# Kernel tuning notes

Hardware: AMD Instinct MI355X
Metric: run time of the kernel (lower is better)

The kernel has to match this reference:

```python
import jax, jax.numpy as jnp
import numpy as np

S, M, E = 8192, 4096, 64          # tokens, model_dim, num_experts
CAPACITY_FACTOR = 1.0
MIN_CAPACITY = 8
CAPACITY = max(int(np.ceil(S / E * CAPACITY_FACTOR)), MIN_CAPACITY)  # 128


def setup_inputs() -> dict:
    key = jax.random.key(0)
    k1, k2 = jax.random.split(key)
    x = jax.random.normal(k1, (S, M), dtype=jnp.float32)
    wg = jax.random.normal(k2, (E, M), dtype=jnp.float32) * (1.0 / np.sqrt(M))
    return {"x": x, "wg": wg}


def reference(x, wg):
    # gate projection (Linear, no bias): logits [s, e]
    logits = jnp.einsum('sm,em->se', x, wg)
    gates = jax.nn.softmax(logits, axis=1)                      # [s, e]

    # top-1 expert per token
    indices1_s = jnp.argmax(gates, axis=1)                      # [s]
    mask1 = jax.nn.one_hot(indices1_s, E, dtype=jnp.int32)      # [s, e]
    exp_counts = jnp.sum(mask1, axis=0)                         # [e]

    # load-balancing aux loss
    me = jnp.mean(gates, axis=0)
    ce = jnp.mean(mask1.astype(jnp.float32), axis=0)
    l_aux = jnp.sum(me * ce) * E

    # capacity drop (use_rts=False): keep first CAPACITY tokens per expert.
    # torch: top_idx = topk(mask1, capacity, dim=0)[1]; scatter ones at those rows.
    top_idx = jax.lax.top_k(mask1.T, CAPACITY)[1]               # [e, c] token ids
    keep = jnp.zeros((S, E), dtype=jnp.int32).at[top_idx.T, jnp.arange(E)[None, :]].set(1)
    mask1 = mask1 * keep                                        # [s, e]

    # position of each token inside its expert's buffer
    locations1 = jnp.cumsum(mask1, axis=0) - 1                  # [s, e]
    locations1_s = jnp.sum(locations1 * mask1, axis=1)          # [s]

    mask1_f = mask1.astype(gates.dtype)
    gates_masked = gates * mask1_f                              # [s, e]
    locations1_sc = jax.nn.one_hot(locations1_s, CAPACITY, dtype=jnp.float32)  # [s, c]

    combine_weights = jnp.einsum('se,sc->sec', gates_masked, locations1_sc)    # [s, e, c]
    dispatch_mask = combine_weights.astype(bool)
    return l_aux, combine_weights, dispatch_mask, exp_counts
```

## Files before the change

### kernel.cpp

```cpp
#include <hip/hip_runtime.h>
#include <hip/hip_bf16.h>

#define TS 8192
#define TM 4096
#define TE 64
#define TCAP 128
static const size_t CW = (size_t)TS * TE * TCAP;
static const size_t OUT_ELEMS = 1 + 2 * CW + TE;
static const size_t OUT_BYTES = OUT_ELEMS * sizeof(float);

#define BM 256
#define BK 16
#define SA 260
#define SW 68

__global__ __launch_bounds__(256) void gemm_partial(
    const float* __restrict__ x, const float* __restrict__ wg,
    float* __restrict__ part, int kchunk) {
  __shared__ float As[BK][SA];
  __shared__ float Ws[BK][SW];
  const int tid = threadIdx.x;
  const int t0 = blockIdx.x * BM;
  const int k0 = blockIdx.y * kchunk;
  const int ntile = kchunk / BK;
  const int tg = tid >> 3;
  const int eg = tid & 7;

  float acc[8][8] = {};
  float4 ra[4]; float4 rw;

  auto load_tile = [&](int kt) {
    const int kb = k0 + kt * BK;
#pragma unroll
    for (int i = 0; i < 4; i++) {
      int idx = tid + 256 * i;
      int tok = idx >> 2, c4 = idx & 3;
      ra[i] = *(const float4*)&x[(size_t)(t0 + tok) * TM + kb + 4 * c4];
    }
    int e = tid >> 2, c4 = tid & 3;
    rw = *(const float4*)&wg[(size_t)e * TM + kb + 4 * c4];
  };

  load_tile(0);
  for (int kt = 0; kt < ntile; kt++) {
#pragma unroll
    for (int i = 0; i < 4; i++) {
      int idx = tid + 256 * i;
      int tok = idx >> 2, c4 = idx & 3;
      As[4 * c4 + 0][tok] = ra[i].x; As[4 * c4 + 1][tok] = ra[i].y;
      As[4 * c4 + 2][tok] = ra[i].z; As[4 * c4 + 3][tok] = ra[i].w;
    }
    { int e = tid >> 2, c4 = tid & 3;
      Ws[4 * c4 + 0][e] = rw.x; Ws[4 * c4 + 1][e] = rw.y;
      Ws[4 * c4 + 2][e] = rw.z; Ws[4 * c4 + 3][e] = rw.w; }
    __syncthreads();
    if (kt + 1 < ntile) load_tile(kt + 1);
#pragma unroll
    for (int k = 0; k < BK; k++) {
      float4 a0 = *(const float4*)&As[k][tg * 8];
      float4 a1 = *(const float4*)&As[k][tg * 8 + 4];
      float4 b0 = *(const float4*)&Ws[k][eg * 8];
      float4 b1 = *(const float4*)&Ws[k][eg * 8 + 4];
      float av[8] = {a0.x, a0.y, a0.z, a0.w, a1.x, a1.y, a1.z, a1.w};
      float bv[8] = {b0.x, b0.y, b0.z, b0.w, b1.x, b1.y, b1.z, b1.w};
#pragma unroll
      for (int i = 0; i < 8; i++)
#pragma unroll
        for (int j = 0; j < 8; j++) acc[i][j] += av[i] * bv[j];
    }
    __syncthreads();
  }
  float* dst = part + (size_t)blockIdx.y * TS * TE;
#pragma unroll
  for (int i = 0; i < 8; i++) {
    int tok = t0 + tg * 8 + i;
#pragma unroll
    for (int j = 0; j < 8; j += 4) {
      float4 v = make_float4(acc[i][j], acc[i][j + 1], acc[i][j + 2], acc[i][j + 3]);
      *(float4*)&dst[(size_t)tok * TE + eg * 8 + j] = v;
    }
  }
}

__global__ __launch_bounds__(256) void softmax_top1(
    const float* __restrict__ part, int KS,
    float* __restrict__ gates, float* __restrict__ gate1, int* __restrict__ idx1) {
  const int s = blockIdx.x * 4 + (threadIdx.x >> 6);
  const int lane = threadIdx.x & 63;
  float logit = 0.0f;
  for (int p = 0; p < KS; p++)
    logit += part[((size_t)p * TS + s) * TE + lane];

  float mv = logit; int mi = lane;
#pragma unroll
  for (int off = 32; off; off >>= 1) {
    float ov = __shfl_xor(mv, off);
    int oi = __shfl_xor(mi, off);
    if (ov > mv || (ov == mv && oi < mi)) { mv = ov; mi = oi; }
  }
  float ex = expf(logit - mv);
  float sum = ex;
#pragma unroll
  for (int off = 32; off; off >>= 1) sum += __shfl_xor(sum, off);
  float g = ex / sum;
  gates[(size_t)s * TE + lane] = g;
  if (lane == mi) { gate1[s] = g; idx1[s] = mi; }
}

__global__ __launch_bounds__(256) void me_reduce(const float* __restrict__ gates,
                                                 float* __restrict__ me) {
  const int e = blockIdx.x, tid = threadIdx.x;
  float s = 0.0f;
  for (int t = tid; t < TS; t += 256) s += gates[(size_t)t * TE + e];
  __shared__ float red[256];
  red[tid] = s; __syncthreads();
  for (int o = 128; o; o >>= 1) { if (tid < o) red[tid] += red[tid + o]; __syncthreads(); }
  if (tid == 0) me[e] = red[0];
}

__global__ void capacity_rank(const int* __restrict__ idx1,
                              int* __restrict__ pos, int* __restrict__ counts) {
  const int e = blockIdx.x, lane = threadIdx.x;
  int base = 0;
  for (int c = 0; c < TS / 64; c++) {
    int s = c * 64 + lane;
    bool m = (idx1[s] == e);
    unsigned long long mask = __ballot(m);
    if (m) {
      int p = base + __popcll(mask & ((1ull << lane) - 1ull));
      pos[s] = (p < TCAP) ? p : -1;
    }
    base += __popcll(mask);
  }
  if (lane == 0) counts[e] = base;
}

__global__ void finalize_laux(const float* __restrict__ me, const int* __restrict__ counts,
                              float* __restrict__ out, size_t cw) {
  const int lane = threadIdx.x;
  float v = (me[lane] / (float)TS) * ((float)counts[lane] / (float)TS);
  float sum = v;
#pragma unroll
  for (int off = 32; off; off >>= 1) sum += __shfl_xor(sum, off);
  if (lane == 0) out[0] = sum * (float)TE;
  out[1 + 2 * cw + lane] = (float)counts[lane];
}

__global__ __launch_bounds__(256) void scatter_out(
    const float* __restrict__ gate1, const int* __restrict__ idx1,
    const int* __restrict__ pos, float* __restrict__ out, size_t cw) {
  const int s = blockIdx.x * 256 + threadIdx.x;
  int p = pos[s];
  if (p >= 0) {
    size_t off = 1 + ((size_t)s * TE + idx1[s]) * (size_t)TCAP + (size_t)p;
    out[off] = gate1[s];
    out[off + cw] = 1.0f;
  }
}

extern "C" void kernel_launch(void* const* d_in, const int* in_sizes, int n_in,
                              void* d_out, int out_size, void* d_ws, size_t ws_size,
                              hipStream_t stream) {
  const float* x = (const float*)d_in[0];
  const float* wg = (const float*)d_in[1];
  float* out = (float*)d_out;

  const size_t SE = (size_t)TS * TE;
  int KS = 8;
  auto need = [&](int ks) {
    return (size_t)ks * SE * 4 + SE * 4 + (size_t)TS * 12 + 1024;
  };
  while (KS > 1 && need(KS) > ws_size) KS >>= 1;

  float* part  = (float*)d_ws;
  float* gates = part + (size_t)KS * SE;
  float* gate1 = gates + SE;
  int*   idx1  = (int*)(gate1 + TS);
  int*   pos   = idx1 + TS;
  float* me    = (float*)(pos + TS);
  int*   cnts  = (int*)(me + TE);

  hipMemsetAsync(d_out, 0, OUT_BYTES, stream);

  dim3 ggrid(TS / BM, KS);
  gemm_partial<<<ggrid, 256, 0, stream>>>(x, wg, part, TM / KS);
  softmax_top1<<<TS / 4, 256, 0, stream>>>(part, KS, gates, gate1, idx1);
  me_reduce<<<TE, 256, 0, stream>>>(gates, me);
  capacity_rank<<<TE, 64, 0, stream>>>(idx1, pos, cnts);
  finalize_laux<<<1, 64, 0, stream>>>(me, cnts, out, CW);
  scatter_out<<<TS / 256, 256, 0, stream>>>(gate1, idx1, pos, out, CW);
}
```

Before: 699.8 us.

## Halve GEMM token tile and fuse small reduction kernels into fewer launches

Shrinks the gate GEMM block tile from 256 to 128 tokens, giving each thread 4x8 outputs. This doubles the grid to fill more CUs and cuts register pressure. It also merges the mean-gate reduction and the capacity ranking into one kernel, and folds the aux-loss finalization into an extra block of the scatter kernel, removing two launches. The cost is that each GEMM block reuses the shared W tile over fewer tokens, and the capacity ranking now runs serially after the reduction inside one block.

```diff
diff --git a/kernel.cpp b/kernel.cpp
--- a/kernel.cpp
+++ b/kernel.cpp
@@ -9,9 +9,9 @@
 static const size_t OUT_ELEMS = 1 + 2 * CW + TE;
 static const size_t OUT_BYTES = OUT_ELEMS * sizeof(float);
 
-#define BM 256
+#define BM 128
 #define BK 16
-#define SA 260
+#define SA 132
 #define SW 68
 
 __global__ __launch_bounds__(256) void gemm_partial(
@@ -26,13 +26,13 @@
   const int tg = tid >> 3;
   const int eg = tid & 7;
 
-  float acc[8][8] = {};
-  float4 ra[4]; float4 rw;
+  float acc[4][8] = {};
+  float4 ra[2]; float4 rw;
 
   auto load_tile = [&](int kt) {
     const int kb = k0 + kt * BK;
 #pragma unroll
-    for (int i = 0; i < 4; i++) {
+    for (int i = 0; i < 2; i++) {
       int idx = tid + 256 * i;
       int tok = idx >> 2, c4 = idx & 3;
       ra[i] = *(const float4*)&x[(size_t)(t0 + tok) * TM + kb + 4 * c4];
@@ -44,7 +44,7 @@
   load_tile(0);
   for (int kt = 0; kt < ntile; kt++) {
 #pragma unroll
-    for (int i = 0; i < 4; i++) {
+    for (int i = 0; i < 2; i++) {
       int idx = tid + 256 * i;
       int tok = idx >> 2, c4 = idx & 3;
       As[4 * c4 + 0][tok] = ra[i].x; As[4 * c4 + 1][tok] = ra[i].y;
@@ -57,14 +57,13 @@
     if (kt + 1 < ntile) load_tile(kt + 1);
 #pragma unroll
     for (int k = 0; k < BK; k++) {
-      float4 a0 = *(const float4*)&As[k][tg * 8];
-      float4 a1 = *(const float4*)&As[k][tg * 8 + 4];
+      float4 a0 = *(const float4*)&As[k][tg * 4];
       float4 b0 = *(const float4*)&Ws[k][eg * 8];
       float4 b1 = *(const float4*)&Ws[k][eg * 8 + 4];
-      float av[8] = {a0.x, a0.y, a0.z, a0.w, a1.x, a1.y, a1.z, a1.w};
+      float av[4] = {a0.x, a0.y, a0.z, a0.w};
       float bv[8] = {b0.x, b0.y, b0.z, b0.w, b1.x, b1.y, b1.z, b1.w};
 #pragma unroll
-      for (int i = 0; i < 8; i++)
+      for (int i = 0; i < 4; i++)
 #pragma unroll
         for (int j = 0; j < 8; j++) acc[i][j] += av[i] * bv[j];
     }
@@ -72,8 +71,8 @@
   }
   float* dst = part + (size_t)blockIdx.y * TS * TE;
 #pragma unroll
-  for (int i = 0; i < 8; i++) {
-    int tok = t0 + tg * 8 + i;
+  for (int i = 0; i < 4; i++) {
+    int tok = t0 + tg * 4 + i;
 #pragma unroll
     for (int j = 0; j < 8; j += 4) {
       float4 v = make_float4(acc[i][j], acc[i][j + 1], acc[i][j + 2], acc[i][j + 3]);
@@ -107,8 +106,9 @@
   if (lane == mi) { gate1[s] = g; idx1[s] = mi; }
 }
 
-__global__ __launch_bounds__(256) void me_reduce(const float* __restrict__ gates,
-                                                 float* __restrict__ me) {
+__global__ __launch_bounds__(256) void stats(
+    const float* __restrict__ gates, const int* __restrict__ idx1,
+    float* __restrict__ me, int* __restrict__ pos, int* __restrict__ counts) {
   const int e = blockIdx.x, tid = threadIdx.x;
   float s = 0.0f;
   for (int t = tid; t < TS; t += 256) s += gates[(size_t)t * TE + e];
@@ -116,39 +116,40 @@
   red[tid] = s; __syncthreads();
   for (int o = 128; o; o >>= 1) { if (tid < o) red[tid] += red[tid + o]; __syncthreads(); }
   if (tid == 0) me[e] = red[0];
-}
 
-__global__ void capacity_rank(const int* __restrict__ idx1,
-                              int* __restrict__ pos, int* __restrict__ counts) {
-  const int e = blockIdx.x, lane = threadIdx.x;
-  int base = 0;
-  for (int c = 0; c < TS / 64; c++) {
-    int s = c * 64 + lane;
-    bool m = (idx1[s] == e);
-    unsigned long long mask = __ballot(m);
-    if (m) {
-      int p = base + __popcll(mask & ((1ull << lane) - 1ull));
-      pos[s] = (p < TCAP) ? p : -1;
+  if (tid < 64) {
+    const int lane = tid;
+    int base = 0;
+    for (int c = 0; c < TS / 64; c++) {
+      int sTok = c * 64 + lane;
+      bool m = (idx1[sTok] == e);
+      unsigned long long mask = __ballot(m);
+      if (m) {
+        int p = base + __popcll(mask & ((1ull << lane) - 1ull));
+        pos[sTok] = (p < TCAP) ? p : -1;
+      }
+      base += __popcll(mask);
     }
-    base += __popcll(mask);
+    if (lane == 0) counts[e] = base;
   }
-  if (lane == 0) counts[e] = base;
-}
-
-__global__ void finalize_laux(const float* __restrict__ me, const int* __restrict__ counts,
-                              float* __restrict__ out, size_t cw) {
-  const int lane = threadIdx.x;
-  float v = (me[lane] / (float)TS) * ((float)counts[lane] / (float)TS);
-  float sum = v;
-#pragma unroll
-  for (int off = 32; off; off >>= 1) sum += __shfl_xor(sum, off);
-  if (lane == 0) out[0] = sum * (float)TE;
-  out[1 + 2 * cw + lane] = (float)counts[lane];
 }
 
 __global__ __launch_bounds__(256) void scatter_out(
     const float* __restrict__ gate1, const int* __restrict__ idx1,
-    const int* __restrict__ pos, float* __restrict__ out, size_t cw) {
+    const int* __restrict__ pos, const float* __restrict__ me,
+    const int* __restrict__ counts, float* __restrict__ out, size_t cw) {
+  if (blockIdx.x == TS / 256) {
+    const int lane = threadIdx.x;
+    if (lane < 64) {
+      float v = (me[lane] / (float)TS) * ((float)counts[lane] / (float)TS);
+      float sum = v;
+#pragma unroll
+      for (int off = 32; off; off >>= 1) sum += __shfl_xor(sum, off);
+      if (lane == 0) out[0] = sum * (float)TE;
+      out[1 + 2 * cw + lane] = (float)counts[lane];
+    }
+    return;
+  }
   const int s = blockIdx.x * 256 + threadIdx.x;
   int p = pos[s];
   if (p >= 0) {
@@ -185,8 +186,6 @@
   dim3 ggrid(TS / BM, KS);
   gemm_partial<<<ggrid, 256, 0, stream>>>(x, wg, part, TM / KS);
   softmax_top1<<<TS / 4, 256, 0, stream>>>(part, KS, gates, gate1, idx1);
-  me_reduce<<<TE, 256, 0, stream>>>(gates, me);
-  capacity_rank<<<TE, 64, 0, stream>>>(idx1, pos, cnts);
-  finalize_laux<<<1, 64, 0, stream>>>(me, cnts, out, CW);
-  scatter_out<<<TS / 256, 256, 0, stream>>>(gate1, idx1, pos, out, CW);
+  stats<<<TE, 256, 0, stream>>>(gates, idx1, me, pos, cnts);
+  scatter_out<<<TS / 256 + 1, 256, 0, stream>>>(gate1, idx1, pos, me, cnts, out, CW);
 }
```

New measurement: 684.2 us. 2.2% less time.
